# Optimization experiments

Hardware: AMD Instinct MI355X
Metric: run time of the kernel (lower is better)

## Reference

```python
import jax, jax.numpy as jnp
import numpy as np

B, N, D_MODEL, N_HEADS, WINDOW = 2, 2048, 1024, 16, 512
HEAD_DIM = D_MODEL // N_HEADS

def setup_inputs() -> dict:
    key = jax.random.key(0)
    k1, k2, k3 = jax.random.split(key, 3)
    x = jax.random.normal(k1, (B, N, D_MODEL), dtype=jnp.float32)
    W_qkv = jax.random.normal(k2, (D_MODEL, 3 * D_MODEL), dtype=jnp.float32) * 0.02
    W_proj = jax.random.normal(k3, (D_MODEL, D_MODEL), dtype=jnp.float32) * 0.02
    b_proj = jnp.zeros((D_MODEL,), dtype=jnp.float32)
    return {"x": x, "W_qkv": W_qkv, "W_proj": W_proj, "b_proj": b_proj}

def reference(x, W_qkv, W_proj, b_proj):
    Bx, Nx, C = x.shape
    H, Dh = N_HEADS, C // N_HEADS
    scale = Dh ** -0.5
    window = min(WINDOW, Nx)
    half = window // 2
    # qkv: [B,N,3C] -> [3,B,H,N,Dh]
    qkv = (x @ W_qkv).reshape(Bx, Nx, 3, H, Dh).transpose(2, 0, 3, 1, 4)
    q, k, v = qkv[0], qkv[1], qkv[2]
    # banded mask: allowed iff i-half <= j <= i+half
    i = jnp.arange(Nx)[:, None]
    j = jnp.arange(Nx)[None, :]
    allowed = jnp.abs(i - j) <= half  # [N,N] bool
    attn = jnp.einsum('bhqd,bhkd->bhqk', q, k) * scale
    attn = jnp.where(allowed[None, None], attn, -jnp.inf)
    attn = jax.nn.softmax(attn, axis=-1)
    out = jnp.einsum('bhqk,bhkd->bhqd', attn, v)
    out = out.transpose(0, 2, 1, 3).reshape(Bx, Nx, C)
    return out @ W_proj + b_proj
```

## Files before the change

kernel.cpp:

```cpp
#include <hip/hip_runtime.h>
#include <stdint.h>


typedef _Float16 f16x8 __attribute__((ext_vector_type(8)));
typedef _Float16 f16x4 __attribute__((ext_vector_type(4)));
typedef __fp16   fp16x2n __attribute__((ext_vector_type(2)));
typedef float    f32x2 __attribute__((ext_vector_type(2)));
typedef float    f32x4 __attribute__((ext_vector_type(4)));
typedef float    f32x16 __attribute__((ext_vector_type(16)));

#define MFMA16(a, b, c) __builtin_amdgcn_mfma_f32_16x16x32_f16((a), (b), (c), 0, 0, 0)
#define MFMA32(a, b, c) __builtin_amdgcn_mfma_f32_32x32x16_f16((a), (b), (c), 0, 0, 0)

__device__ __forceinline__ void gload16(const void* g, void* l) {
  __builtin_amdgcn_global_load_lds(
      (const __attribute__((address_space(1))) void*)g,
      (__attribute__((address_space(3))) void*)l, 16, 0, 0);
}

__device__ __forceinline__ unsigned pk2(float a, float b) {
  fp16x2n t = __builtin_amdgcn_cvt_pkrtz(a, b);
  return __builtin_bit_cast(unsigned, t);
}

__global__ __launch_bounds__(256) void prep(const float* __restrict__ x,
                                            const float* __restrict__ wqkv,
                                            const float* __restrict__ wproj,
                                            _Float16* __restrict__ Xb,
                                            _Float16* __restrict__ Wqt,
                                            _Float16* __restrict__ Wpt) {
  __shared__ float t[64][65];
  const int id = blockIdx.x, tid = threadIdx.x;
  if (id < 4096) {
    int i = (id * 256 + tid) * 4;
    float4 v = *(const float4*)(x + i);
    f16x4 h;
    h[0] = (_Float16)v.x; h[1] = (_Float16)v.y;
    h[2] = (_Float16)v.z; h[3] = (_Float16)v.w;
    *(f16x4*)(Xb + i) = h;
    return;
  }
  const float* in; _Float16* out; int N, bx, by;
  if (id < 4864) { int tt = id - 4096; in = wqkv; out = Wqt; N = 3072; bx = tt % 48; by = tt / 48; }
  else           { int tt = id - 4864; in = wproj; out = Wpt; N = 1024; bx = tt & 15; by = tt >> 4; }
  const int n0 = bx * 64, k0 = by * 64;
  {
    int j = tid & 63;
#pragma unroll
    for (int p = 0; p < 16; p++) {
      int i = p * 4 + (tid >> 6);
      t[i][j] = in[(size_t)(k0 + i) * N + n0 + j];
    }
  }
  __syncthreads();
  {
    int i = tid & 63;
#pragma unroll
    for (int p = 0; p < 16; p++) {
      int j = p * 4 + (tid >> 6);
      out[(size_t)(n0 + j) * 1024 + k0 + i] = (_Float16)t[i][j];
    }
  }
}

__global__ __launch_bounds__(512) void gemm8p(const _Float16* __restrict__ A,
                                              const _Float16* __restrict__ Bt,
                                              _Float16* __restrict__ oh,
                                              _Float16* __restrict__ vt) {
  __shared__ __align__(16) char smem[147456];
  const int tid = threadIdx.x, wave = tid >> 6, lane = tid & 63;
  const int il = lane & 15, ih = lane >> 4;
  const int rs = lane >> 3, cp = lane & 7;
  const int bm = blockIdx.y * 256, bn = blockIdx.x * 192;
  const int wm = wave >> 2, wn = wave & 3;
  const int srow = wave * 8 + rs;

#define R15_STAGE_A(ABUF, T)                                                  \
  _Pragma("unroll") for (int hh = 0; hh < 4; hh++) {                          \
    int row = hh * 64 + srow;                                                 \
    int c = cp ^ (row & 7);                                                   \
    gload16(A + (size_t)(bm + row) * 1024 + (T) * 64 + c * 8,                 \
            smem + (ABUF) * 32768 + hh * 8192 + wave * 1024);                 \
  }
#define R15_STAGE_B(BBUF, T)                                                  \
  _Pragma("unroll") for (int hh = 0; hh < 3; hh++) {                          \
    int row = hh * 64 + srow;                                                 \
    int c = cp ^ (row & 7);                                                   \
    gload16(Bt + (size_t)(bn + row) * 1024 + (T) * 64 + c * 8,                \
            smem + 98304 + (BBUF) * 24576 + hh * 8192 + wave * 1024);         \
  }

  f32x4 acc[8][3] = {};

  R15_STAGE_A(0, 0);
  R15_STAGE_B(0, 0);
  R15_STAGE_A(1, 1);
  R15_STAGE_B(1, 1);
  asm volatile("s_waitcnt vmcnt(7)" ::: "memory");
  __builtin_amdgcn_s_barrier();

  int ta = 0, sa = 2;
#pragma unroll 1
  for (int t = 0; t < 16; t++) {
    const char* Abuf = (const char*)smem + ta * 32768;
    const char* Bbuf = (const char*)smem + 98304 + (t & 1) * 24576;
    f16x8 af[4][2], ag[4][2], bf[3][2];
#pragma unroll
    for (int m = 0; m < 4; m++) {
      int R = wm * 128 + m * 16 + il;
#pragma unroll
      for (int ks = 0; ks < 2; ks++)
        af[m][ks] = *(const f16x8*)(Abuf + R * 128 + (((ks * 4 + ih) ^ (R & 7)) * 16));
    }
#pragma unroll
    for (int n = 0; n < 3; n++) {
      int C = wn * 48 + n * 16 + il;
#pragma unroll
      for (int ks = 0; ks < 2; ks++)
        bf[n][ks] = *(const f16x8*)(Bbuf + C * 128 + (((ks * 4 + ih) ^ (C & 7)) * 16));
    }
    if (t < 14) { R15_STAGE_A(sa, t + 2); }
    asm volatile("s_waitcnt lgkmcnt(0)" ::: "memory");
    __builtin_amdgcn_s_barrier();
    __builtin_amdgcn_s_setprio(1);
#pragma unroll
    for (int m = 0; m < 4; m++)
#pragma unroll
      for (int n = 0; n < 3; n++)
#pragma unroll
        for (int ks = 0; ks < 2; ks++)
          acc[m][n] = MFMA16(af[m][ks], bf[n][ks], acc[m][n]);
    __builtin_amdgcn_s_setprio(0);
#pragma unroll
    for (int m = 0; m < 4; m++) {
      int R = wm * 128 + 64 + m * 16 + il;
#pragma unroll
      for (int ks = 0; ks < 2; ks++)
        ag[m][ks] = *(const f16x8*)(Abuf + R * 128 + (((ks * 4 + ih) ^ (R & 7)) * 16));
    }
    if (t < 14) { R15_STAGE_B(t & 1, t + 2); }
    __builtin_amdgcn_s_setprio(1);
#pragma unroll
    for (int m = 0; m < 4; m++)
#pragma unroll
      for (int n = 0; n < 3; n++)
#pragma unroll
        for (int ks = 0; ks < 2; ks++)
          acc[4 + m][n] = MFMA16(ag[m][ks], bf[n][ks], acc[4 + m][n]);
    __builtin_amdgcn_s_setprio(0);
    if (t <= 13) {
      asm volatile("s_waitcnt vmcnt(7)" ::: "memory");
    } else if (t == 14) {
      asm volatile("s_waitcnt vmcnt(0)" ::: "memory");
    }
    if (t < 15) __builtin_amdgcn_s_barrier();
    ta = (ta == 2) ? 0 : ta + 1;
    sa = (sa == 2) ? 0 : sa + 1;
  }

#pragma unroll
  for (int mi = 0; mi < 8; mi++)
#pragma unroll
    for (int ni = 0; ni < 3; ni++) {
      int row0 = bm + wm * 128 + mi * 16 + ih * 4;
      int col = bn + wn * 48 + ni * 16 + il;
      int sec = col >> 10, cc = col & 1023;
      if (sec == 2) {
        int b = row0 >> 11, n = row0 & 2047;
        int bh2 = b * 16 + (cc >> 6), dh = cc & 63;
        union { f16x4 h; uint2 u; } pk;
#pragma unroll
        for (int r = 0; r < 4; r++) pk.h[r] = (_Float16)acc[mi][ni][r];
        *(uint2*)(vt + (size_t)bh2 * 131072 + (size_t)dh * 2048 + n) = pk.u;
      } else {
#pragma unroll
        for (int r = 0; r < 4; r++) {
          int row = row0 + r;
          float v = acc[mi][ni][r];
          if (sec == 0) v *= 0.18033688f;
          size_t plane = (size_t)(sec * 32 + (row >> 11) * 16 + (cc >> 6));
          oh[plane * 131072 + (size_t)(row & 2047) * 64 + (cc & 63)] = (_Float16)v;
        }
      }
    }
#undef R15_STAGE_A
#undef R15_STAGE_B
}

__global__ __launch_bounds__(512) void gemm2p(const _Float16* __restrict__ A,
                                              const _Float16* __restrict__ Bt,
                                              float* __restrict__ of,
                                              const float* __restrict__ bias) {
  __shared__ __align__(16) char smem[81920];
  const int tid = threadIdx.x, wave = tid >> 6, lane = tid & 63;
  const int il = lane & 15, ih = lane >> 4;
  const int rs = lane >> 3, cp = lane & 7;
  const int bm = blockIdx.y * 128, bn = blockIdx.x * 128;
  const int wm = wave >> 2, wn = wave & 3;
  const int srow = wave * 8 + rs;

#define R17_STAGE_A(ABUF, T)                                                  \
  _Pragma("unroll") for (int hh = 0; hh < 2; hh++) {                          \
    int row = hh * 64 + srow;                                                 \
    int c = cp ^ (row & 7);                                                   \
    gload16(A + (size_t)(bm + row) * 1024 + (T) * 64 + c * 8,                 \
            smem + (ABUF) * 16384 + hh * 8192 + wave * 1024);                 \
  }
#define R17_STAGE_B(BBUF, T)                                                  \
  _Pragma("unroll") for (int hh = 0; hh < 2; hh++) {                          \
    int row = hh * 64 + srow;                                                 \
    int c = cp ^ (row & 7);                                                   \
    gload16(Bt + (size_t)(bn + row) * 1024 + (T) * 64 + c * 8,                \
            smem + 49152 + (BBUF) * 16384 + hh * 8192 + wave * 1024);         \
  }

  f32x4 acc[4][2] = {};

  R17_STAGE_A(0, 0);
  R17_STAGE_B(0, 0);
  R17_STAGE_A(1, 1);
  R17_STAGE_B(1, 1);
  asm volatile("s_waitcnt vmcnt(4)" ::: "memory");
  __builtin_amdgcn_s_barrier();

  int ta = 0, sa = 2;
#pragma unroll 1
  for (int t = 0; t < 16; t++) {
    const char* Abuf = (const char*)smem + ta * 16384;
    const char* Bbuf = (const char*)smem + 49152 + (t & 1) * 16384;
    f16x8 af[4][2], bf[2][2];
#pragma unroll
    for (int m = 0; m < 4; m++) {
      int R = wm * 64 + m * 16 + il;
#pragma unroll
      for (int ks = 0; ks < 2; ks++)
        af[m][ks] = *(const f16x8*)(Abuf + R * 128 + (((ks * 4 + ih) ^ (R & 7)) * 16));
    }
#pragma unroll
    for (int n = 0; n < 2; n++) {
      int C = wn * 32 + n * 16 + il;
#pragma unroll
      for (int ks = 0; ks < 2; ks++)
        bf[n][ks] = *(const f16x8*)(Bbuf + C * 128 + (((ks * 4 + ih) ^ (C & 7)) * 16));
    }
    if (t < 14) { R17_STAGE_A(sa, t + 2); }
    asm volatile("s_waitcnt lgkmcnt(0)" ::: "memory");
    __builtin_amdgcn_s_barrier();
    if (t < 14) { R17_STAGE_B(t & 1, t + 2); }
    __builtin_amdgcn_s_setprio(1);
#pragma unroll
    for (int m = 0; m < 4; m++)
#pragma unroll
      for (int n = 0; n < 2; n++)
#pragma unroll
        for (int ks = 0; ks < 2; ks++)
          acc[m][n] = MFMA16(af[m][ks], bf[n][ks], acc[m][n]);
    __builtin_amdgcn_s_setprio(0);
    if (t <= 13) {
      asm volatile("s_waitcnt vmcnt(4)" ::: "memory");
    } else if (t == 14) {
      asm volatile("s_waitcnt vmcnt(0)" ::: "memory");
    }
    if (t < 15) __builtin_amdgcn_s_barrier();
    ta = (ta == 2) ? 0 : ta + 1;
    sa = (sa == 2) ? 0 : sa + 1;
  }

#pragma unroll
  for (int mi = 0; mi < 4; mi++)
#pragma unroll
    for (int ni = 0; ni < 2; ni++) {
      int row0 = bm + wm * 64 + mi * 16 + ih * 4;
      int col = bn + wn * 32 + ni * 16 + il;
#pragma unroll
      for (int r = 0; r < 4; r++)
        of[(size_t)(row0 + r) * 1024 + col] = acc[mi][ni][r] + bias[col];
    }
#undef R17_STAGE_A
#undef R17_STAGE_B
}

__global__ __launch_bounds__(512) void attn(const _Float16* __restrict__ QKV,
                                            const _Float16* __restrict__ VT,
                                            _Float16* __restrict__ O2) {
  __shared__ __align__(16) char smem[51200];
  const int tid = threadIdx.x, wave = tid >> 6, lane = tid & 63;
  const int qw = wave >> 1, sh = wave & 1;
  const int cl = lane & 31, hl = lane >> 5;
  const int rs = lane >> 3, cp = lane & 7;
  const int q0 = blockIdx.x * 128, bh = blockIdx.y;
  const _Float16* Qg = QKV + (size_t)bh * 131072;
  const _Float16* Kg = QKV + 4194304 + (size_t)bh * 131072;
  const _Float16* Vg = VT + (size_t)bh * 131072;
  const int t0 = (q0 >= 256) ? q0 - 256 : 0;
  const int t1 = (q0 + 384 <= 2048) ? q0 + 384 : 2048;
  const int niter = (t1 - t0) >> 6;

#pragma unroll
  for (int q = 0; q < 2; q++) {
    int s = 2 * wave + q;
    int row = s * 8 + rs;
    int c = cp ^ (row & 7);
    gload16(Qg + (size_t)(q0 + row) * 64 + c * 8, smem + s * 1024);
  }
  {
    char* B0 = smem + 18432;
    int row = wave * 8 + rs;
    int c = cp ^ (row & 7);
    gload16(Kg + (size_t)(t0 + row) * 64 + c * 8, B0 + wave * 1024);
    gload16(Vg + (size_t)row * 2048 + t0 + c * 8, B0 + 8192 + wave * 1024);
  }
  __syncthreads();

  f16x8 bq[4];
  {
    int row = 32 * qw + cl;
#pragma unroll
    for (int ks = 0; ks < 4; ks++)
      bq[ks] = *(const f16x8*)(smem + row * 128 + (((ks * 2 + hl) ^ (row & 7)) * 16));
  }

  f32x16 oacc[2] = {};
  float l_acc = 0.f;
  const int a0 = q0 + 32 * qw;

  for (int i = 0; i < niter; i++) {
    const int kt = t0 + i * 64;
    char* Bc = smem + 18432 + (i & 1) * 16384;
    if (i + 1 < niter) {
      char* Bn = smem + 18432 + ((i + 1) & 1) * 16384;
      int row = wave * 8 + rs;
      int c = cp ^ (row & 7);
      gload16(Kg + (size_t)(kt + 64 + row) * 64 + c * 8, Bn + wave * 1024);
      gload16(Vg + (size_t)row * 2048 + (kt + 64) + c * 8, Bn + 8192 + wave * 1024);
    }
    const int d0 = a0 - (kt + 32 * sh);
    if (d0 < 288 && d0 > -288) {
      char* Ksm = Bc;
      char* Vsm = Bc + 8192;
      f32x16 st = {};
      {
        const int krow = 32 * sh + cl;
        __builtin_amdgcn_s_setprio(1);
#pragma unroll
        for (int ks = 0; ks < 4; ks++) {
          f16x8 ak = *(const f16x8*)(Ksm + krow * 128 + (((ks * 2 + hl) ^ (krow & 7)) * 16));
          st = MFMA32(ak, bq[ks], st);
        }
        __builtin_amdgcn_s_setprio(0);
      }
      unsigned w0a[4], w1a[4];
#pragma unroll
      for (int g = 0; g < 4; g++) {
        float v[4];
#pragma unroll
        for (int i2 = 0; i2 < 4; i2++) {
          float e = __builtin_amdgcn_exp2f(st[4 * g + i2]);
          int kl = 8 * g + 4 * hl + i2;
          if (d0 == 256) e = (cl <= kl) ? e : 0.f;
          else if (d0 == -256) e = (cl >= kl) ? e : 0.f;
          l_acc += e;
          v[i2] = e;
        }
        w0a[g] = pk2(v[0], v[1]);
        w1a[g] = pk2(v[2], v[3]);
      }
#pragma unroll
      for (int ks2 = 0; ks2 < 2; ks2++) {
        unsigned kA0 = w0a[2 * ks2],     kA1 = w1a[2 * ks2];
        unsigned kB0 = w0a[2 * ks2 + 1], kB1 = w1a[2 * ks2 + 1];
        unsigned keep0 = hl ? kB0 : kA0, keep1 = hl ? kB1 : kA1;
        unsigned send0 = hl ? kA0 : kB0, send1 = hl ? kA1 : kB1;
        unsigned r0 = (unsigned)__shfl_xor((int)send0, 32);
        unsigned r1 = (unsigned)__shfl_xor((int)send1, 32);
        union { unsigned u[4]; f16x8 h; } bp;
        bp.u[0] = hl ? r0 : keep0;
        bp.u[1] = hl ? r1 : keep1;
        bp.u[2] = hl ? keep0 : r0;
        bp.u[3] = hl ? keep1 : r1;
        __builtin_amdgcn_s_setprio(1);
#pragma unroll
        for (int db = 0; db < 2; db++) {
          int vrow = 32 * db + cl;
          f16x8 av = *(const f16x8*)(Vsm + vrow * 128 +
                                     (((4 * sh + 2 * ks2 + hl) ^ (vrow & 7)) * 16));
          oacc[db] = MFMA32(av, bp.h, oacc[db]);
        }
        __builtin_amdgcn_s_setprio(0);
      }
    }
    __syncthreads();
  }

  const float lp = l_acc + __shfl_xor(l_acc, 32);
  char* Mq = smem + qw * 8448;
  if (sh == 1) {
#pragma unroll
    for (int db = 0; db < 2; db++)
#pragma unroll
      for (int g = 0; g < 4; g++) {
        int dh0 = 32 * db + 8 * g + 4 * hl;
        f32x2 a = {oacc[db][4 * g + 0], oacc[db][4 * g + 1]};
        f32x2 b = {oacc[db][4 * g + 2], oacc[db][4 * g + 3]};
        *(f32x2*)(Mq + cl * 264 + dh0 * 4) = a;
        *(f32x2*)(Mq + cl * 264 + dh0 * 4 + 8) = b;
      }
    if (hl == 0) *(float*)(smem + 34816 + (qw * 32 + cl) * 4) = lp;
  }
  __syncthreads();
  if (sh == 0) {
    float lo = *(const float*)(smem + 34816 + (qw * 32 + cl) * 4);
    float inv = 1.0f / (lp + lo);
    const int b = bh >> 4, h = bh & 15;
    _Float16* dst = O2 + (size_t)(b * 2048 + a0 + cl) * 1024 + h * 64;
#pragma unroll
    for (int db = 0; db < 2; db++)
#pragma unroll
      for (int g = 0; g < 4; g++) {
        int dh0 = 32 * db + 8 * g + 4 * hl;
        f32x2 a = *(const f32x2*)(Mq + cl * 264 + dh0 * 4);
        f32x2 b2 = *(const f32x2*)(Mq + cl * 264 + dh0 * 4 + 8);
        uint2 pkd = {pk2((oacc[db][4 * g + 0] + a[0]) * inv,
                         (oacc[db][4 * g + 1] + a[1]) * inv),
                     pk2((oacc[db][4 * g + 2] + b2[0]) * inv,
                         (oacc[db][4 * g + 3] + b2[1]) * inv)};
        *(uint2*)(dst + dh0) = pkd;
      }
  }
}


extern "C" void kernel_launch(void* const* d_in, const int* in_sizes, int n_in,
                              void* d_out, int out_size, void* d_ws, size_t ws_size,
                              hipStream_t stream) {
  const float* x = (const float*)d_in[0];
  const float* wqkv = (const float*)d_in[1];
  const float* wproj = (const float*)d_in[2];
  const float* bproj = (const float*)d_in[3];
  float* out = (float*)d_out;
  char* ws = (char*)d_ws;

  _Float16* Xb  = (_Float16*)(ws);
  _Float16* Wqt = (_Float16*)(ws + (size_t)(8  << 20));
  _Float16* Wpt = (_Float16*)(ws + (size_t)(14 << 20));
  _Float16* QKV = (_Float16*)(ws + (size_t)(16 << 20));
  _Float16* Vt  = (_Float16*)(ws + (size_t)(40 << 20));
  _Float16* O2  = (_Float16*)(ws);

  prep<<<5120, 256, 0, stream>>>(x, wqkv, wproj, Xb, Wqt, Wpt);
  gemm8p<<<dim3(16, 16), 512, 0, stream>>>(Xb, Wqt, QKV, Vt);
  attn<<<dim3(16, 32), 512, 0, stream>>>(QKV, Vt, O2);
  gemm2p<<<dim3(8, 32), 512, 0, stream>>>(O2, Wpt, out, bproj);
}
```

Measured before the change: 154.3 us.

## Triple-buffer K/V tiles in attention with two-ahead prefetch and partial vmcnt waits

Changes the attention kernel's K/V staging from double to triple buffering, reusing the Q region to fit within 48KB of shared memory. Two tiles are prefetched ahead, and the full __syncthreads is replaced by an s_waitcnt vmcnt(2) plus a raw barrier, so the next tile's loads can stay in flight across the barrier. This aims to hide global-to-LDS latency better. In exchange it adds manual wait-count reasoning, which could race if the compiler emits other vector memory ops inside the loop.

```diff
diff --git a/kernel.cpp b/kernel.cpp
--- a/kernel.cpp
+++ b/kernel.cpp
@@ -283,7 +283,7 @@
 __global__ __launch_bounds__(512) void attn(const _Float16* __restrict__ QKV,
                                             const _Float16* __restrict__ VT,
                                             _Float16* __restrict__ O2) {
-  __shared__ __align__(16) char smem[51200];
+  __shared__ __align__(16) char smem[49152];
   const int tid = threadIdx.x, wave = tid >> 6, lane = tid & 63;
   const int qw = wave >> 1, sh = wave & 1;
   const int cl = lane & 31, hl = lane >> 5;
@@ -295,21 +295,20 @@
   const int t0 = (q0 >= 256) ? q0 - 256 : 0;
   const int t1 = (q0 + 384 <= 2048) ? q0 + 384 : 2048;
   const int niter = (t1 - t0) >> 6;
+  const int srow = wave * 8 + rs;
+  const int sc = cp ^ (srow & 7);
 
 #pragma unroll
   for (int q = 0; q < 2; q++) {
     int s = 2 * wave + q;
     int row = s * 8 + rs;
     int c = cp ^ (row & 7);
-    gload16(Qg + (size_t)(q0 + row) * 64 + c * 8, smem + s * 1024);
-  }
-  {
-    char* B0 = smem + 18432;
-    int row = wave * 8 + rs;
-    int c = cp ^ (row & 7);
-    gload16(Kg + (size_t)(t0 + row) * 64 + c * 8, B0 + wave * 1024);
-    gload16(Vg + (size_t)row * 2048 + t0 + c * 8, B0 + 8192 + wave * 1024);
-  }
+    gload16(Qg + (size_t)(q0 + row) * 64 + c * 8, smem + 32768 + s * 1024);
+  }
+  gload16(Kg + (size_t)(t0 + srow) * 64 + sc * 8, smem + wave * 1024);
+  gload16(Vg + (size_t)srow * 2048 + t0 + sc * 8, smem + 8192 + wave * 1024);
+  gload16(Kg + (size_t)(t0 + 64 + srow) * 64 + sc * 8, smem + 16384 + wave * 1024);
+  gload16(Vg + (size_t)srow * 2048 + (t0 + 64) + sc * 8, smem + 16384 + 8192 + wave * 1024);
   __syncthreads();
 
   f16x8 bq[4];
@@ -317,27 +316,27 @@
     int row = 32 * qw + cl;
 #pragma unroll
     for (int ks = 0; ks < 4; ks++)
-      bq[ks] = *(const f16x8*)(smem + row * 128 + (((ks * 2 + hl) ^ (row & 7)) * 16));
-  }
+      bq[ks] = *(const f16x8*)(smem + 32768 + row * 128 + (((ks * 2 + hl) ^ (row & 7)) * 16));
+  }
+  asm volatile("s_waitcnt lgkmcnt(0)" ::: "memory");
+  __builtin_amdgcn_s_barrier();
 
   f32x16 oacc[2] = {};
   float l_acc = 0.f;
   const int a0 = q0 + 32 * qw;
 
+  int bc = 0, bs = 2;
   for (int i = 0; i < niter; i++) {
     const int kt = t0 + i * 64;
-    char* Bc = smem + 18432 + (i & 1) * 16384;
-    if (i + 1 < niter) {
-      char* Bn = smem + 18432 + ((i + 1) & 1) * 16384;
-      int row = wave * 8 + rs;
-      int c = cp ^ (row & 7);
-      gload16(Kg + (size_t)(kt + 64 + row) * 64 + c * 8, Bn + wave * 1024);
-      gload16(Vg + (size_t)row * 2048 + (kt + 64) + c * 8, Bn + 8192 + wave * 1024);
+    if (i + 2 < niter) {
+      char* Bn = smem + bs * 16384;
+      gload16(Kg + (size_t)(kt + 128 + srow) * 64 + sc * 8, Bn + wave * 1024);
+      gload16(Vg + (size_t)srow * 2048 + (kt + 128) + sc * 8, Bn + 8192 + wave * 1024);
     }
     const int d0 = a0 - (kt + 32 * sh);
     if (d0 < 288 && d0 > -288) {
-      char* Ksm = Bc;
-      char* Vsm = Bc + 8192;
+      char* Ksm = smem + bc * 16384;
+      char* Vsm = Ksm + 8192;
       f32x16 st = {};
       {
         const int krow = 32 * sh + cl;
@@ -389,8 +388,16 @@
         __builtin_amdgcn_s_setprio(0);
       }
     }
-    __syncthreads();
-  }
+    if (i + 2 < niter) {
+      asm volatile("s_waitcnt vmcnt(2)" ::: "memory");
+    } else {
+      asm volatile("s_waitcnt vmcnt(0)" ::: "memory");
+    }
+    __builtin_amdgcn_s_barrier();
+    bc = (bc == 2) ? 0 : bc + 1;
+    bs = (bs == 2) ? 0 : bs + 1;
+  }
+  __syncthreads();
 
   const float lp = l_acc + __shfl_xor(l_acc, 32);
   char* Mq = smem + qw * 8448;
```

New measurement: 155.6 us. Within noise of the previous version (+0.9%).
